# Kernel optimization log

Hardware: AMD Instinct MI355X
Metric: run time of the kernel (lower is better)

Reference implementation:

```python
import jax, jax.numpy as jnp
import numpy as np

NUM_EMB = 1024
EMB_DIM = 256
BETA = 0.25


def setup_inputs() -> dict:
    key = jax.random.key(0)
    k1, k2 = jax.random.split(key)
    z = jax.random.normal(k1, (64, 32, 32, EMB_DIM), dtype=jnp.float32)
    # RandomUniform(-1/N, 1/N) init, shape (embedding_dimension, number_embeddings)
    embeddings = jax.random.uniform(
        k2, (EMB_DIM, NUM_EMB), dtype=jnp.float32,
        minval=-1.0 / NUM_EMB, maxval=1.0 / NUM_EMB)
    return {"z": z, "embeddings": embeddings}


def reference(z, embeddings):
    beta = BETA
    z_flat = z.reshape(-1, EMB_DIM)                      # [N, D]
    # squared L2 distances via ||z||^2 + ||e||^2 - 2 z @ e
    distances = (jnp.sum(z_flat ** 2, axis=1, keepdims=True)
                 + jnp.sum(embeddings ** 2, axis=0)
                 - 2.0 * (z_flat @ embeddings))          # [N, K]
    encoding_indices = jnp.argmin(distances, axis=1)     # [N] int
    quantized = embeddings.T[encoding_indices].reshape(z.shape)  # gather rows of e^T
    vq_loss = jnp.mean((quantized - jax.lax.stop_gradient(z)) ** 2)
    commitment_loss = beta * jnp.mean((jax.lax.stop_gradient(quantized) - z) ** 2)
    quantized_st = z + jax.lax.stop_gradient(quantized - z)  # straight-through
    # perplexity from codebook usage histogram
    counts = jnp.zeros((NUM_EMB,), dtype=distances.dtype).at[encoding_indices].add(1.0)
    avg_probs = counts / encoding_indices.shape[0]
    perplexity = jnp.exp(-jnp.sum(avg_probs * jnp.log(avg_probs + 1e-10)))
    return (quantized_st, encoding_indices, vq_loss, commitment_loss, perplexity)
```

## Files before the change

### kernel.cpp

```cpp
#include <hip/hip_runtime.h>
#include <math.h>

#define NUM_EMB 1024
#define EMB_DIM 256
#define NROWS   65536
#define NTHREADS 256
#define MTHREADS 1024
#define EPSF 1.5e-3f
#define GCAP 524288

#define OFF_IDX  16777216
#define OFF_VQ   16842752

#define WS_C2    0
#define WS_HIST  4096
#define WS_LOSS  8192
#define WS_GCNT  8196
#define WS_R2    8448
#define WS_SLOT  270592
#define WS_ETF   794880
#define WS_ETB   1843456
#define WS_GLIST 2367744

typedef __attribute__((ext_vector_type(8))) short bf16x8;
typedef __attribute__((ext_vector_type(4))) float f32x4;

__device__ __forceinline__ unsigned short f2bf(float x) {
  unsigned u = __float_as_uint(x);
  unsigned r = (u + 0x7FFFu + ((u >> 16) & 1u)) >> 16;
  return (unsigned short)r;
}

__global__ __launch_bounds__(NTHREADS) void vq_prep(
    const float* __restrict__ emb, float* __restrict__ cvec,
    int* __restrict__ hist, float* __restrict__ loss, int* __restrict__ gcnt) {
  int k = blockIdx.x * blockDim.x + threadIdx.x;
  if (k < NUM_EMB) {
    float s = 0.f;
    for (int d = 0; d < EMB_DIM; ++d) {
      float v = emb[d * NUM_EMB + k];
      s = __fadd_rn(s, __fmul_rn(v, v));
    }
    cvec[k] = s;
    hist[k] = 0;
  }
  if (k == 0) { *loss = 0.f; *gcnt = 0; }
}

__global__ __launch_bounds__(NTHREADS) void vq_tr(
    const float* __restrict__ emb, float* __restrict__ embTf,
    unsigned short* __restrict__ embTbf) {
  __shared__ float t[64][65];
  const int kt = blockIdx.x & 15, dt = blockIdx.x >> 4;
  const int tid = threadIdx.x;
  #pragma unroll
  for (int it = 0; it < 16; ++it) {
    int i = tid + it * NTHREADS, r = i >> 6, c = i & 63;
    t[r][c] = emb[(dt * 64 + r) * NUM_EMB + kt * 64 + c];
  }
  __syncthreads();
  #pragma unroll
  for (int it = 0; it < 16; ++it) {
    int i = tid + it * NTHREADS, r = i >> 6, c = i & 63;
    float v = t[c][r];
    embTf[(kt * 64 + r) * EMB_DIM + dt * 64 + c] = v;
    embTbf[(kt * 64 + r) * EMB_DIM + dt * 64 + c] = f2bf(v);
  }
}

__global__ __launch_bounds__(NTHREADS) void vq_r2k(
    const float* __restrict__ z, float* __restrict__ r2out) {
  __shared__ float zc[64][36];
  __shared__ float pmm[64][2][4];
  const int tid = threadIdx.x;
  const int n0 = blockIdx.x * 64;
  const float* zrow = z + (size_t)n0 * EMB_DIM;
  const int prow = tid >> 2, pm = tid & 3;
  float racc[2][2] = {{0.f, 0.f}, {0.f, 0.f}};
  for (int dc = 0; dc < 8; ++dc) {
    __syncthreads();
    #pragma unroll
    for (int it = 0; it < 2; ++it) {
      int i = tid + it * NTHREADS, row = i >> 3, f4 = i & 7;
      *(float4*)(&zc[row][f4 * 4]) = *(const float4*)(zrow + row * EMB_DIM + dc * 32 + f4 * 4);
    }
    __syncthreads();
    const int half = dc >> 2;
    #pragma unroll
    for (int q = 0; q < 4; ++q)
      #pragma unroll
      for (int jj = 0; jj < 2; ++jj) {
        float v = zc[prow][(pm * 2 + jj) + 8 * q];
        racc[half][jj] = __fadd_rn(racc[half][jj], __fmul_rn(v, v));
      }
  }
  pmm[prow][0][pm] = __fadd_rn(racc[0][0], racc[0][1]);
  pmm[prow][1][pm] = __fadd_rn(racc[1][0], racc[1][1]);
  __syncthreads();
  if (tid < 64) {
    float h0 = __fadd_rn(__fadd_rn(pmm[tid][0][0], pmm[tid][0][1]),
                         __fadd_rn(pmm[tid][0][2], pmm[tid][0][3]));
    float h1 = __fadd_rn(__fadd_rn(pmm[tid][1][0], pmm[tid][1][1]),
                         __fadd_rn(pmm[tid][1][2], pmm[tid][1][3]));
    r2out[n0 + tid] = __fadd_rn(h0, h1);
  }
}

__global__ __launch_bounds__(MTHREADS) void vq_mfma(
    const float* __restrict__ z, const unsigned short* __restrict__ embTbf,
    const float* __restrict__ cvec, unsigned long long* __restrict__ slots,
    int* __restrict__ gcnt, unsigned int* __restrict__ glist) {
  __shared__ unsigned short zc[256][256];
  __shared__ unsigned short Bl[256][40];
  __shared__ int rowminb[256];
  __shared__ unsigned int llist[2048];
  __shared__ int lcnt, lbase, lcount;

  const int tid = threadIdx.x;
  const int lane = tid & 63, wave = tid >> 6;
  const int quad = lane >> 4, l15 = lane & 15;
  const int rg = wave >> 2, cg = wave & 3;
  const int n0 = blockIdx.x * 256;

  if (tid < 256) {
    rowminb[tid] = 0x7F000000;
    slots[n0 + tid] = ~0ULL;
  }

  #pragma unroll
  for (int it = 0; it < 8; ++it) {
    int g = tid + it * MTHREADS, row = g >> 5, u = g & 31;
    const float* src = z + (size_t)(n0 + row) * EMB_DIM + u * 8;
    float4 a = *(const float4*)src;
    float4 b = *(const float4*)(src + 4);
    uint4 w;
    w.x = ((unsigned)f2bf(a.y) << 16) | f2bf(a.x);
    w.y = ((unsigned)f2bf(a.w) << 16) | f2bf(a.z);
    w.z = ((unsigned)f2bf(b.y) << 16) | f2bf(b.x);
    w.w = ((unsigned)f2bf(b.w) << 16) | f2bf(b.z);
    *(uint4*)(&zc[row][(u ^ (row & 7)) * 8]) = w;
  }

  const int bn = tid >> 2, bseg = tid & 3;
  const size_t bofs = (size_t)bn * EMB_DIM + (size_t)bseg * 8;
  uint4 bpre = *(const uint4*)(embTbf + bofs);

  for (int j = 0; j < 4; ++j) {
    f32x4 acc[4][4];
    #pragma unroll
    for (int rt = 0; rt < 4; ++rt)
      #pragma unroll
      for (int ct = 0; ct < 4; ++ct)
        acc[rt][ct] = (f32x4){0.f, 0.f, 0.f, 0.f};
    float c2r[4];
    #pragma unroll
    for (int ct = 0; ct < 4; ++ct)
      c2r[ct] = cvec[j * 256 + cg * 64 + ct * 16 + l15] + 1.0f;

    for (int kc = 0; kc < 8; ++kc) {
      __syncthreads();
      *(uint4*)(&Bl[bn][bseg * 8]) = bpre;
      __syncthreads();
      int c = j * 8 + kc + 1;
      if (c < 32)
        bpre = *(const uint4*)(embTbf + (size_t)(c >> 3) * 65536 +
                               (size_t)(c & 7) * 32 + bofs);
      bf16x8 av[4], bv[4];
      #pragma unroll
      for (int rt = 0; rt < 4; ++rt) {
        int row = rg * 64 + rt * 16 + l15;
        av[rt] = *(const bf16x8*)(&zc[row][((kc * 4 + quad) ^ (l15 & 7)) * 8]);
      }
      #pragma unroll
      for (int ct = 0; ct < 4; ++ct)
        bv[ct] = *(const bf16x8*)(&Bl[cg * 64 + ct * 16 + l15][quad * 8]);
      #pragma unroll
      for (int rt = 0; rt < 4; ++rt)
        #pragma unroll
        for (int ct = 0; ct < 4; ++ct)
          acc[rt][ct] = __builtin_amdgcn_mfma_f32_16x16x32_bf16(av[rt], bv[ct], acc[rt][ct], 0, 0, 0);
    }

    #pragma unroll
    for (int rt = 0; rt < 4; ++rt)
      #pragma unroll
      for (int reg = 0; reg < 4; ++reg) {
        float m = 1e30f;
        #pragma unroll
        for (int ct = 0; ct < 4; ++ct) {
          float d = fmaf(-2.f, acc[rt][ct][reg], c2r[ct]);
          m = fminf(m, d);
        }
        #pragma unroll
        for (int off = 1; off < 16; off <<= 1)
          m = fminf(m, __shfl_xor(m, off));
        if (l15 == 0)
          atomicMin(&rowminb[rg * 64 + rt * 16 + quad * 4 + reg], __float_as_int(m));
      }
    if (tid == 0) lcnt = 0;
    __syncthreads();

    #pragma unroll
    for (int rt = 0; rt < 4; ++rt)
      #pragma unroll
      for (int reg = 0; reg < 4; ++reg) {
        int rowl = rg * 64 + rt * 16 + quad * 4 + reg;
        float fmin = __int_as_float(rowminb[rowl]);
        #pragma unroll
        for (int ct = 0; ct < 4; ++ct) {
          int k = j * 256 + cg * 64 + ct * 16 + l15;
          float d = fmaf(-2.f, acc[rt][ct][reg], c2r[ct]);
          if (d <= fmin + EPSF) {
            int id = atomicAdd(&lcnt, 1);
            if (id < 2048) llist[id] = ((unsigned)(n0 + rowl) << 10) | (unsigned)k;
          }
        }
      }
    __syncthreads();
    if (tid == 0) {
      int c = lcnt < 2048 ? lcnt : 2048;
      lcount = c;
      lbase = atomicAdd(gcnt, c);
    }
    __syncthreads();
    for (int i = tid; i < lcount; i += MTHREADS)
      if (lbase + i < GCAP) glist[lbase + i] = llist[i];
    __syncthreads();
  }
}

__global__ __launch_bounds__(NTHREADS) void vq_refine(
    const float* __restrict__ z, const float* __restrict__ embTf,
    const float* __restrict__ r2, const float* __restrict__ cvec,
    const int* __restrict__ gcnt, const unsigned int* __restrict__ glist,
    unsigned long long* __restrict__ slots) {
  int n = *gcnt; if (n > GCAP) n = GCAP;
  for (int i = blockIdx.x * NTHREADS + threadIdx.x; i < n;
       i += gridDim.x * NTHREADS) {
    unsigned e = glist[i];
    int grow = (int)(e >> 10), k = (int)(e & 1023);
    const float* zr = z + (size_t)grow * EMB_DIM;
    const float* er = embTf + (size_t)k * EMB_DIM;
    float s = 0.f;
    for (int d = 0; d < EMB_DIM; ++d)
      s = fmaf(zr[d], er[d], s);
    float dist = __fsub_rn(__fadd_rn(r2[grow], cvec[k]), __fmul_rn(2.0f, s));
    unsigned long long key =
        ((unsigned long long)__float_as_uint(dist) << 32) | (unsigned)k;
    atomicMin(&slots[grow], key);
  }
}

__global__ __launch_bounds__(NTHREADS) void vq_epi(
    const float* __restrict__ z, const float* __restrict__ embTf,
    const unsigned long long* __restrict__ slots,
    float* __restrict__ out, int* __restrict__ hist, float* __restrict__ loss) {
  __shared__ int ks[64];
  __shared__ float wsum[4];
  const int tid = threadIdx.x;
  const int n0 = blockIdx.x * 64;
  const float* zrow = z + (size_t)n0 * EMB_DIM;
  if (tid < 64) {
    int k = (int)(slots[n0 + tid] & 1023ULL);
    ks[tid] = k;
    out[OFF_IDX + n0 + tid] = (float)k;
    atomicAdd(&hist[k], 1);
  }
  __syncthreads();
  float sumsq = 0.f;
  #pragma unroll
  for (int it = 0; it < 16; ++it) {
    int g = tid + it * NTHREADS;
    int row = g >> 6;
    int d = (g & 63) * 4;
    int k = ks[row];
    float4 zv = *(const float4*)(zrow + row * EMB_DIM + d);
    float4 q = *(const float4*)(embTf + (size_t)k * EMB_DIM + d);
    float4 df;
    df.x = q.x - zv.x; df.y = q.y - zv.y; df.z = q.z - zv.z; df.w = q.w - zv.w;
    sumsq = fmaf(df.x, df.x, sumsq);
    sumsq = fmaf(df.y, df.y, sumsq);
    sumsq = fmaf(df.z, df.z, sumsq);
    sumsq = fmaf(df.w, df.w, sumsq);
    *(float4*)(out + (size_t)(n0 + row) * EMB_DIM + d) = q;
  }
  #pragma unroll
  for (int off = 32; off > 0; off >>= 1) sumsq += __shfl_down(sumsq, off);
  if ((tid & 63) == 0) wsum[tid >> 6] = sumsq;
  __syncthreads();
  if (tid == 0) atomicAdd(loss, wsum[0] + wsum[1] + wsum[2] + wsum[3]);
}

__global__ __launch_bounds__(NTHREADS) void vq_finalize(
    const int* __restrict__ hist, const float* __restrict__ loss,
    float* __restrict__ out) {
  __shared__ float ws[4];
  int tid = threadIdx.x;
  float s = 0.f;
  for (int k = tid; k < NUM_EMB; k += NTHREADS) {
    float p = (float)hist[k] * (1.0f / 65536.0f);
    s += p * logf(p + 1e-10f);
  }
  #pragma unroll
  for (int off = 32; off > 0; off >>= 1) s += __shfl_down(s, off);
  if ((tid & 63) == 0) ws[tid >> 6] = s;
  __syncthreads();
  if (tid == 0) {
    float tot = ws[0] + ws[1] + ws[2] + ws[3];
    float vq = *loss * (1.0f / 16777216.0f);
    out[OFF_VQ + 0] = vq;
    out[OFF_VQ + 1] = 0.25f * vq;
    out[OFF_VQ + 2] = expf(-tot);
  }
}

extern "C" void kernel_launch(void* const* d_in, const int* in_sizes, int n_in,
                              void* d_out, int out_size, void* d_ws, size_t ws_size,
                              hipStream_t stream) {
  const float* z   = (const float*)d_in[0];
  const float* emb = (const float*)d_in[1];
  float* out = (float*)d_out;
  char* ws = (char*)d_ws;
  float* cvec   = (float*)(ws + WS_C2);
  int*   hist   = (int*)(ws + WS_HIST);
  float* loss   = (float*)(ws + WS_LOSS);
  int*   gcnt   = (int*)(ws + WS_GCNT);
  float* r2     = (float*)(ws + WS_R2);
  unsigned long long* slots = (unsigned long long*)(ws + WS_SLOT);
  float* embTf  = (float*)(ws + WS_ETF);
  unsigned short* embTbf = (unsigned short*)(ws + WS_ETB);
  unsigned int* glist = (unsigned int*)(ws + WS_GLIST);

  vq_prep<<<4, NTHREADS, 0, stream>>>(emb, cvec, hist, loss, gcnt);
  vq_tr<<<64, NTHREADS, 0, stream>>>(emb, embTf, embTbf);
  vq_r2k<<<NROWS / 64, NTHREADS, 0, stream>>>(z, r2);
  vq_mfma<<<NROWS / 256, MTHREADS, 0, stream>>>(z, embTbf, cvec, slots, gcnt, glist);
  vq_refine<<<512, NTHREADS, 0, stream>>>(z, embTf, r2, cvec, gcnt, glist, slots);
  vq_epi<<<NROWS / 64, NTHREADS, 0, stream>>>(z, embTf, slots, out, hist, loss);
  vq_finalize<<<1, NTHREADS, 0, stream>>>(hist, loss, out);
}
```

Measured before the change: 291.1 us.

## Fuse prep and transpose kernels; read MFMA B operand directly from global

Merges the codebook-norm prep kernel and the transpose kernel into one launch with block-index dispatch, saving a launch. In the MFMA kernel, the B tile is no longer staged through shared memory with a register prefetch and two barriers per k-chunk. Each wave now loads its bf16 codebook fragments straight from global memory (which is L2-resident) and the inner loop is unrolled by two. This removes per-iteration syncs and LDS traffic, but the B loads are now uncoalesced and duplicated across the four row-group waves.

Measured after the change: 301.3 us. +3.5%, slower.

```diff
diff --git a/kernel.cpp b/kernel.cpp
--- a/kernel.cpp
+++ b/kernel.cpp
@@ -31,11 +31,14 @@
   return (unsigned short)r;
 }
 
-__global__ __launch_bounds__(NTHREADS) void vq_prep(
+__global__ __launch_bounds__(NTHREADS) void vq_pt(
     const float* __restrict__ emb, float* __restrict__ cvec,
-    int* __restrict__ hist, float* __restrict__ loss, int* __restrict__ gcnt) {
-  int k = blockIdx.x * blockDim.x + threadIdx.x;
-  if (k < NUM_EMB) {
+    int* __restrict__ hist, float* __restrict__ loss, int* __restrict__ gcnt,
+    float* __restrict__ embTf, unsigned short* __restrict__ embTbf) {
+  __shared__ float t[64][65];
+  const int tid = threadIdx.x;
+  if (blockIdx.x < 4) {
+    int k = blockIdx.x * NTHREADS + tid;
     float s = 0.f;
     for (int d = 0; d < EMB_DIM; ++d) {
       float v = emb[d * NUM_EMB + k];
@@ -43,28 +46,23 @@
     }
     cvec[k] = s;
     hist[k] = 0;
-  }
-  if (k == 0) { *loss = 0.f; *gcnt = 0; }
-}
-
-__global__ __launch_bounds__(NTHREADS) void vq_tr(
-    const float* __restrict__ emb, float* __restrict__ embTf,
-    unsigned short* __restrict__ embTbf) {
-  __shared__ float t[64][65];
-  const int kt = blockIdx.x & 15, dt = blockIdx.x >> 4;
-  const int tid = threadIdx.x;
-  #pragma unroll
-  for (int it = 0; it < 16; ++it) {
-    int i = tid + it * NTHREADS, r = i >> 6, c = i & 63;
-    t[r][c] = emb[(dt * 64 + r) * NUM_EMB + kt * 64 + c];
-  }
-  __syncthreads();
-  #pragma unroll
-  for (int it = 0; it < 16; ++it) {
-    int i = tid + it * NTHREADS, r = i >> 6, c = i & 63;
-    float v = t[c][r];
-    embTf[(kt * 64 + r) * EMB_DIM + dt * 64 + c] = v;
-    embTbf[(kt * 64 + r) * EMB_DIM + dt * 64 + c] = f2bf(v);
+    if (k == 0) { *loss = 0.f; *gcnt = 0; }
+  } else {
+    const int b = blockIdx.x - 4;
+    const int kt = b & 15, dt = b >> 4;
+    #pragma unroll
+    for (int it = 0; it < 16; ++it) {
+      int i = tid + it * NTHREADS, r = i >> 6, c = i & 63;
+      t[r][c] = emb[(dt * 64 + r) * NUM_EMB + kt * 64 + c];
+    }
+    __syncthreads();
+    #pragma unroll
+    for (int it = 0; it < 16; ++it) {
+      int i = tid + it * NTHREADS, r = i >> 6, c = i & 63;
+      float v = t[c][r];
+      embTf[(kt * 64 + r) * EMB_DIM + dt * 64 + c] = v;
+      embTbf[(kt * 64 + r) * EMB_DIM + dt * 64 + c] = f2bf(v);
+    }
   }
 }
 
@@ -111,7 +109,6 @@
     const float* __restrict__ cvec, unsigned long long* __restrict__ slots,
     int* __restrict__ gcnt, unsigned int* __restrict__ glist) {
   __shared__ unsigned short zc[256][256];
-  __shared__ unsigned short Bl[256][40];
   __shared__ int rowminb[256];
   __shared__ unsigned int llist[2048];
   __shared__ int lcnt, lbase, lcount;
@@ -140,10 +137,7 @@
     w.w = ((unsigned)f2bf(b.w) << 16) | f2bf(b.z);
     *(uint4*)(&zc[row][(u ^ (row & 7)) * 8]) = w;
   }
-
-  const int bn = tid >> 2, bseg = tid & 3;
-  const size_t bofs = (size_t)bn * EMB_DIM + (size_t)bseg * 8;
-  uint4 bpre = *(const uint4*)(embTbf + bofs);
+  __syncthreads();
 
   for (int j = 0; j < 4; ++j) {
     f32x4 acc[4][4];
@@ -157,14 +151,8 @@
     for (int ct = 0; ct < 4; ++ct)
       c2r[ct] = cvec[j * 256 + cg * 64 + ct * 16 + l15] + 1.0f;
 
+    #pragma unroll 2
     for (int kc = 0; kc < 8; ++kc) {
-      __syncthreads();
-      *(uint4*)(&Bl[bn][bseg * 8]) = bpre;
-      __syncthreads();
-      int c = j * 8 + kc + 1;
-      if (c < 32)
-        bpre = *(const uint4*)(embTbf + (size_t)(c >> 3) * 65536 +
-                               (size_t)(c & 7) * 32 + bofs);
       bf16x8 av[4], bv[4];
       #pragma unroll
       for (int rt = 0; rt < 4; ++rt) {
@@ -173,7 +161,9 @@
       }
       #pragma unroll
       for (int ct = 0; ct < 4; ++ct)
-        bv[ct] = *(const bf16x8*)(&Bl[cg * 64 + ct * 16 + l15][quad * 8]);
+        bv[ct] = *(const bf16x8*)(embTbf +
+                   (size_t)(j * 256 + cg * 64 + ct * 16 + l15) * EMB_DIM +
+                   kc * 32 + quad * 8);
       #pragma unroll
       for (int rt = 0; rt < 4; ++rt)
         #pragma unroll
@@ -331,8 +321,7 @@
   unsigned short* embTbf = (unsigned short*)(ws + WS_ETB);
   unsigned int* glist = (unsigned int*)(ws + WS_GLIST);
 
-  vq_prep<<<4, NTHREADS, 0, stream>>>(emb, cvec, hist, loss, gcnt);
-  vq_tr<<<64, NTHREADS, 0, stream>>>(emb, embTf, embTbf);
+  vq_pt<<<68, NTHREADS, 0, stream>>>(emb, cvec, hist, loss, gcnt, embTf, embTbf);
   vq_r2k<<<NROWS / 64, NTHREADS, 0, stream>>>(z, r2);
   vq_mfma<<<NROWS / 256, MTHREADS, 0, stream>>>(z, embTbf, cvec, slots, gcnt, glist);
   vq_refine<<<512, NTHREADS, 0, stream>>>(z, embTf, r2, cvec, gcnt, glist, slots);
```
